# Performance work log

Measured on AMD Instinct MI355X. Metric: run time of the kernel, lower is better.

Reference implementation:

```python
import jax, jax.numpy as jnp
import numpy as np

D_MODEL = 1024
D_STATE = 128
HEADDIM = 64
EXPAND = 2
CHUNK = 64
D_CONV = 4
D_INNER = EXPAND * D_MODEL          # 2048
NHEADS = D_INNER // HEADDIM         # 32
D_IN_PROJ = 2 * D_INNER + 2 * D_STATE + NHEADS  # 4384
CONV_CH = D_INNER + 2 * D_STATE     # 2304
EPS = 1e-5


def segsum(x):
    # x: (..., T) -> (..., T, T); out[i, j] = sum_{k=j+1..i} x[k] for i>=j else -inf
    T = x.shape[-1]
    m1 = jnp.tril(jnp.ones((T, T), bool), -1)
    xr = jnp.where(m1, x[..., :, None], 0.0)   # zero above/at diagonal before cumsum
    s = jnp.cumsum(xr, axis=-2)
    m0 = jnp.tril(jnp.ones((T, T), bool), 0)
    return jnp.where(m0, s, -jnp.inf)


def ssd(x, A, B, C, chunk):
    # x: (b, L, h, p); A: (b, L, h); B, C: (b, L, n)  (the h=1 dim of the torch code is squeezed)
    b, L, h, p = x.shape
    c = L // chunk
    x = x.reshape(b, c, chunk, h, p)
    A = A.reshape(b, c, chunk, h).transpose(0, 3, 1, 2)  # (b, h, c, l)
    B = B.reshape(b, c, chunk, -1)                       # (b, c, l, n)
    C = C.reshape(b, c, chunk, -1)
    A_cum = jnp.cumsum(A, axis=-1)                       # (b, h, c, l)
    Lm = jnp.exp(segsum(A))                              # (b, h, c, l, l)
    # intra-chunk (diagonal block) output
    Y_diag = jnp.einsum('bcln,bcsn,bhcls,bcshp->bclhp', C, B, Lm, x)
    # per-chunk states
    decay_states = jnp.exp(A_cum[:, :, :, -1:] - A_cum)  # (b, h, c, l)
    states = jnp.einsum('bcln,bhcl,bclhp->bchpn', B, decay_states, x)
    init = jnp.zeros_like(states[:, :1])
    states = jnp.concatenate([init, states], axis=1)     # (b, c+1, h, p, n)
    # inter-chunk recurrence
    Ac_last = jnp.pad(A_cum[:, :, :, -1], ((0, 0), (0, 0), (1, 0)))  # (b, h, c+1)
    decay_chunk = jnp.exp(segsum(Ac_last))               # (b, h, c+1, c+1)
    new_states = jnp.einsum('bhzc,bchpn->bzhpn', decay_chunk, states)
    states = new_states[:, :-1]                          # (b, c, h, p, n)
    sdo = jnp.exp(A_cum)
    Y_off = jnp.einsum('bcln,bchpn,bhcl->bclhp', C, states, sdo)
    return (Y_diag + Y_off).reshape(b, L, h, p)


def setup_inputs() -> dict:
    key = jax.random.key(0)
    ks = jax.random.split(key, 8)
    return {
        'u': jax.random.normal(ks[0], (2, 4096, D_MODEL), jnp.float32),
        'W_in': jax.random.normal(ks[1], (D_MODEL, D_IN_PROJ), jnp.float32) * 0.02,
        'conv_w': jax.random.normal(ks[2], (CONV_CH, D_CONV), jnp.float32) * 0.3,
        'conv_b': jax.random.normal(ks[3], (CONV_CH,), jnp.float32) * 0.1,
        'dt_bias': jax.random.normal(ks[4], (NHEADS,), jnp.float32),
        'A_log': jax.random.normal(ks[5], (NHEADS,), jnp.float32) * 0.5,
        'D': jax.random.normal(ks[6], (NHEADS,), jnp.float32),
        'norm_w': jnp.ones((D_INNER,), jnp.float32),
        'W_out': jax.random.normal(ks[7], (D_INNER, D_MODEL), jnp.float32) * 0.02,
    }


def reference(u, W_in, conv_w, conv_b, dt_bias, A_log, D, norm_w, W_out):
    b, L, _ = u.shape
    zxbcdt = u @ W_in                                    # (b, L, 4384)
    z = zxbcdt[..., :D_INNER]
    xBC = zxbcdt[..., D_INNER:D_INNER + CONV_CH]
    dt = jax.nn.softplus(zxbcdt[..., -NHEADS:] + dt_bias)  # (b, L, h)
    # depthwise causal conv (Conv1d pad=d_conv-1, truncated to L == left-pad only)
    xc = jnp.pad(xBC.transpose(0, 2, 1), ((0, 0), (0, 0), (D_CONV - 1, 0)))
    xc = jax.lax.conv_general_dilated(
        xc, conv_w[:, None, :], (1,), 'VALID',
        feature_group_count=CONV_CH,
        dimension_numbers=('NCH', 'OIH', 'NCH')) + conv_b[None, :, None]
    xBC = jax.nn.silu(xc.transpose(0, 2, 1))             # (b, L, 2304)
    x = xBC[..., :D_INNER].reshape(b, L, NHEADS, HEADDIM)
    B = xBC[..., D_INNER:D_INNER + D_STATE]
    C = xBC[..., D_INNER + D_STATE:]
    A = -jnp.exp(A_log)                                  # (h,)
    y = ssd(x * dt[..., None], A * dt, B, C, CHUNK)
    y = y + x * D[:, None]
    y = y.reshape(b, L, D_INNER)
    # RMSNorm with gate z
    y = y * jax.nn.silu(z)
    y = y * jax.lax.rsqrt(jnp.mean(y * y, axis=-1, keepdims=True) + EPS) * norm_w
    return y @ W_out
```

## Files before the change

kernel.cpp:

```cpp
#include <hip/hip_runtime.h>
#include <hip/hip_bf16.h>
#include <math.h>

#define D_MODEL   1024
#define D_STATE   128
#define HEADDIM   64
#define CHUNK     64
#define D_INNER   2048
#define NHEADS    32
#define D_IN_PROJ 4384
#define CONV_CH   2304
#define RCOLS     2336
#define WINT_ROWS 4480
#define BATCH     2
#define SEQ       4096
#define NCHUNK    64
#define ROWS      (BATCH*SEQ)
#define EPS_RMS   1e-5f

typedef __hip_bfloat16 bf16;
typedef __bf16 bf16x8_t __attribute__((ext_vector_type(8)));
typedef float  f32x4_t  __attribute__((ext_vector_type(4)));

__device__ __forceinline__ float siluf_(float x){ return x/(1.f+expf(-x)); }
__device__ __forceinline__ float ldf(const float* p){ return *p; }
__device__ __forceinline__ float ldf(const bf16* p){ return __bfloat162float(*p); }
__device__ __forceinline__ void  stf(float* p, float v){ *p = v; }
__device__ __forceinline__ void  stf(bf16* p, float v){ *p = __float2bfloat16(v); }

__device__ __forceinline__ __bf16 tobf(float v){
    __hip_bfloat16 t = __float2bfloat16(v);
    return *reinterpret_cast<__bf16*>(&t);
}
__device__ __forceinline__ unsigned short bfbits(float v){
    __hip_bfloat16 t = __float2bfloat16(v);
    return *reinterpret_cast<unsigned short*>(&t);
}
__device__ __forceinline__ float bfbits2f(unsigned short u){
    union { unsigned u; float f; } cv; cv.u = ((unsigned)u) << 16; return cv.f;
}

__device__ __forceinline__ void async16(const void* g, void* l) {
    __builtin_amdgcn_global_load_lds(
        (const __attribute__((address_space(1))) unsigned int*)g,
        (__attribute__((address_space(3))) unsigned int*)l, 16, 0, 0);
}

struct Core {
    f32x4_t acc[4][4];

    __device__ __forceinline__ void stageA(const bf16* __restrict__ A, int lda,
                                           int row0, int kk, __bf16* Asb,
                                           int tid, int lcb, int wb) {
#pragma unroll
        for (int c = 0; c < 4; ++c) {
            const char* src = (const char*)(A + (size_t)(row0 + c * 64 + (tid >> 3)) * lda + kk) + lcb;
            async16(src, Asb + c * 4096 + wb);
        }
    }
    __device__ __forceinline__ void stageB(const bf16* __restrict__ Bt, int ldb,
                                           int col0, int kk, __bf16* Bsb,
                                           int tid, int lcb, int wb) {
#pragma unroll
        for (int c = 0; c < 2; ++c) {
            const char* src = (const char*)(Bt + (size_t)(col0 + c * 64 + (tid >> 3)) * ldb + kk) + lcb;
            async16(src, Bsb + c * 4096 + wb);
        }
    }

    __device__ __forceinline__ void run(const bf16* __restrict__ A,
                                        const bf16* __restrict__ Bt,
                                        int lda, int ldb,
                                        int row0, int col0, int k0, int nt,
                                        __bf16* As, __bf16* Bs, int tid) {
        const int wave = tid >> 6, lane = tid & 63;
        const int quad = lane >> 4, l16 = lane & 15;
        const int wm = wave >> 1, wn = wave & 1;
        const int wb  = wave << 9;
        const int lcb = (((tid & 7) ^ ((tid >> 3) & 7)) << 4);
        const int xb = (l16 & 7) << 4;

#pragma unroll
        for (int i = 0; i < 4; ++i)
#pragma unroll
            for (int j = 0; j < 4; ++j) acc[i][j] = (f32x4_t){0.f, 0.f, 0.f, 0.f};

        int aoff[4][2], boff[4][2];
#pragma unroll
        for (int mi = 0; mi < 4; ++mi)
#pragma unroll
            for (int ks = 0; ks < 2; ++ks) {
                const int cb = ((ks << 6) | (quad << 4)) ^ xb;
                aoff[mi][ks] = (wm * 64 + mi * 16 + l16) * 128 + cb;
                boff[mi][ks] = (wn * 64 + mi * 16 + l16) * 128 + cb;
            }

        stageA(A, lda, row0, k0,      As,          tid, lcb, wb);
        stageB(Bt, ldb, col0, k0,     Bs,          tid, lcb, wb);
        stageA(A, lda, row0, k0 + 64, As + 16384,  tid, lcb, wb);
        stageB(Bt, ldb, col0, k0 + 64, Bs + 8192,  tid, lcb, wb);

        const char* AsC = (const char*)As;
        const char* BsC = (const char*)Bs;
        int cur = 0, sb = 2;
        for (int t = 0; t < nt; ++t) {
            if (t < nt - 1) asm volatile("s_waitcnt vmcnt(6)" ::: "memory");
            else            asm volatile("s_waitcnt vmcnt(0)" ::: "memory");
            __builtin_amdgcn_s_barrier();
            asm volatile("" ::: "memory");
            if (t + 2 < nt) {
                stageA(A, lda, row0, k0 + (t + 2) * 64, As + sb * 16384, tid, lcb, wb);
                stageB(Bt, ldb, col0, k0 + (t + 2) * 64, Bs + sb * 8192, tid, lcb, wb);
            }
            const char* Ab = AsC + cur * 32768;
            const char* Bb = BsC + cur * 16384;
            bf16x8_t af[4][2], bfr[4][2];
#pragma unroll
            for (int mi = 0; mi < 4; ++mi)
#pragma unroll
                for (int ks = 0; ks < 2; ++ks) {
                    af[mi][ks]  = *(const bf16x8_t*)(Ab + aoff[mi][ks]);
                    bfr[mi][ks] = *(const bf16x8_t*)(Bb + boff[mi][ks]);
                }
            __builtin_amdgcn_s_setprio(1);
#pragma unroll
            for (int ks = 0; ks < 2; ++ks)
#pragma unroll
                for (int mi = 0; mi < 4; ++mi)
#pragma unroll
                    for (int ni = 0; ni < 4; ++ni)
                        acc[mi][ni] = __builtin_amdgcn_mfma_f32_16x16x32_bf16(
                            af[mi][ks], bfr[ni][ks], acc[mi][ni], 0, 0, 0);
            __builtin_amdgcn_s_setprio(0);
            cur = (cur + 1 == 3) ? 0 : cur + 1;
            sb  = (sb  + 1 == 3) ? 0 : sb  + 1;
        }
    }
};

__global__ __launch_bounds__(512) void gemm_zr_fused(const bf16* __restrict__ A,
                                                     const bf16* __restrict__ Bt,
                                                     bf16* __restrict__ Z,
                                                     bf16* __restrict__ R) {
    __shared__ __align__(16) __bf16 As[3 * 16384];
    __shared__ __align__(16) __bf16 Bs[3 * 8192];
    const int tid = threadIdx.x;
    const int row0 = blockIdx.x * 256;
    const int ct   = blockIdx.y;
    Core g;
    g.run(A, Bt, D_MODEL, D_MODEL, row0, ct * 128, 0, 16, As, Bs, tid);

    const int wave = tid >> 6, lane = tid & 63;
    const int quad = lane >> 4, l16 = lane & 15;
    const int wm = wave >> 1, wn = wave & 1;
    bf16* Cp; int ldc_, cl0, ncols;
    if (ct < 16) { Cp = Z; ldc_ = D_INNER; cl0 = ct * 128;           ncols = D_INNER; }
    else         { Cp = R; ldc_ = RCOLS;   cl0 = ct * 128 - D_INNER; ncols = RCOLS; }
#pragma unroll
    for (int ni = 0; ni < 4; ++ni) {
        int gc = cl0 + wn * 64 + ni * 16 + l16;
        if (gc >= ncols) continue;
#pragma unroll
        for (int mi = 0; mi < 4; ++mi)
#pragma unroll
            for (int r = 0; r < 4; ++r) {
                int gr = row0 + wm * 64 + mi * 16 + quad * 4 + r;
                stf(&Cp[(size_t)gr * ldc_ + gc], g.acc[mi][ni][r]);
            }
    }
}

__global__ __launch_bounds__(512) void gemm_out_kernel(const bf16* __restrict__ A,
                                                       const bf16* __restrict__ Bt,
                                                       float* __restrict__ out) {
    __shared__ __align__(16) __bf16 As[3 * 16384];
    __shared__ __align__(16) __bf16 Bs[3 * 8192];
    const int tid = threadIdx.x;
    const int row0 = blockIdx.x * 256;
    const int col0 = blockIdx.y * 128;
    Core g;
    g.run(A, Bt, D_INNER, D_INNER, row0, col0, 0, 32, As, Bs, tid);

    const int wave = tid >> 6, lane = tid & 63;
    const int quad = lane >> 4, l16 = lane & 15;
    const int wm = wave >> 1, wn = wave & 1;
#pragma unroll
    for (int ni = 0; ni < 4; ++ni) {
        int gc = col0 + wn * 64 + ni * 16 + l16;
#pragma unroll
        for (int mi = 0; mi < 4; ++mi)
#pragma unroll
            for (int r = 0; r < 4; ++r) {
                int gr = row0 + wm * 64 + mi * 16 + quad * 4 + r;
                out[(size_t)gr * D_MODEL + gc] = g.acc[mi][ni][r];
            }
    }
}

__global__ void cvt_bf16_kernel(const float* __restrict__ src,
                                bf16* __restrict__ dst, int n4) {
    int i = blockIdx.x * 256 + threadIdx.x;
    if (i >= n4) return;
    float4 v = ((const float4*)src)[i];
    dst[i * 4 + 0] = __float2bfloat16(v.x);
    dst[i * 4 + 1] = __float2bfloat16(v.y);
    dst[i * 4 + 2] = __float2bfloat16(v.z);
    dst[i * 4 + 3] = __float2bfloat16(v.w);
}

__global__ __launch_bounds__(256) void transpose_cvt_kernel(const float* __restrict__ W,
                                                            bf16* __restrict__ Wt,
                                                            int R, int C, int Cpad) {
    __shared__ float tile[32][33];
    int c0 = blockIdx.x * 32, r0 = blockIdx.y * 32;
    int tx = threadIdx.x & 31, ty = threadIdx.x >> 5;
    for (int i = ty; i < 32; i += 8) {
        int r = r0 + i, c = c0 + tx;
        tile[i][tx] = (c < C) ? W[(size_t)r * C + c] : 0.f;
    }
    __syncthreads();
    for (int i = ty; i < 32; i += 8) {
        int c = c0 + i, r = r0 + tx;
        stf(&Wt[(size_t)c * R + r], tile[tx][i]);
    }
}

__global__ void prep_convw_kernel(const float* __restrict__ conv_w,
                                  bf16* __restrict__ Wc) {
    int i = blockIdx.x * 256 + threadIdx.x;
    if (i >= CONV_CH * 4) return;
    int ch = i >> 2, k = i & 3;
    Wc[k * CONV_CH + ch] = __float2bfloat16(conv_w[ch * 4 + k]);
}

__global__ __launch_bounds__(256) void conv_silu_kernel(const bf16* __restrict__ R,
                                                        const bf16* __restrict__ Wc,
                                                        const float* __restrict__ conv_b,
                                                        bf16* __restrict__ xBC) {
    int idx = blockIdx.x * 256 + threadIdx.x;
    int rq = idx / 288;
    int g = idx - rq * 288;
    int ch0 = g * 8;
    int row0 = rq * 4;
    int l0 = row0 & (SEQ - 1);

    uint4 rv[7];
#pragma unroll
    for (int j = 0; j < 7; ++j) {
        int ls = l0 - 3 + j;
        rv[j] = (ls >= 0) ? *(const uint4*)&R[(size_t)(row0 - 3 + j) * RCOLS + ch0]
                          : make_uint4(0u, 0u, 0u, 0u);
    }
    uint4 wv[4];
#pragma unroll
    for (int k = 0; k < 4; ++k)
        wv[k] = *(const uint4*)&Wc[k * CONV_CH + ch0];
    float4 b0 = ((const float4*)conv_b)[ch0 / 4];
    float4 b1 = ((const float4*)conv_b)[ch0 / 4 + 1];
    const float bias[8] = {b0.x, b0.y, b0.z, b0.w, b1.x, b1.y, b1.z, b1.w};
    float wf[4][8];
#pragma unroll
    for (int k = 0; k < 4; ++k) {
        const unsigned* wp = (const unsigned*)&wv[k];
#pragma unroll
        for (int j2 = 0; j2 < 4; ++j2) {
            wf[k][2 * j2]     = bfbits2f((unsigned short)(wp[j2] & 0xffff));
            wf[k][2 * j2 + 1] = bfbits2f((unsigned short)(wp[j2] >> 16));
        }
    }
#pragma unroll
    for (int j = 0; j < 4; ++j) {
        float acc[8];
#pragma unroll
        for (int cc = 0; cc < 8; ++cc) acc[cc] = bias[cc];
#pragma unroll
        for (int k = 0; k < 4; ++k) {
            const unsigned* vp = (const unsigned*)&rv[j + k];
#pragma unroll
            for (int j2 = 0; j2 < 4; ++j2) {
                unsigned v = vp[j2];
                acc[2 * j2]     += wf[k][2 * j2]     * bfbits2f((unsigned short)(v & 0xffff));
                acc[2 * j2 + 1] += wf[k][2 * j2 + 1] * bfbits2f((unsigned short)(v >> 16));
            }
        }
        unsigned o[4];
#pragma unroll
        for (int j2 = 0; j2 < 4; ++j2)
            o[j2] = (unsigned)bfbits(siluf_(acc[2 * j2])) |
                    ((unsigned)bfbits(siluf_(acc[2 * j2 + 1])) << 16);
        *(uint4*)&xBC[(size_t)(row0 + j) * CONV_CH + ch0] = make_uint4(o[0], o[1], o[2], o[3]);
    }
}

__global__ void dt_kernel(const bf16* __restrict__ R,
                          const float* __restrict__ dt_bias,
                          float* __restrict__ dtb) {
    int i = blockIdx.x * 256 + threadIdx.x;
    int row = i >> 2, h0 = (i & 3) * 8;
    uint4 v = *(const uint4*)&R[(size_t)row * RCOLS + CONV_CH + h0];
    float4 bia0 = ((const float4*)dt_bias)[h0 / 4];
    float4 bia1 = ((const float4*)dt_bias)[h0 / 4 + 1];
    const unsigned vv[4] = {v.x, v.y, v.z, v.w};
    const float bb[8] = {bia0.x, bia0.y, bia0.z, bia0.w, bia1.x, bia1.y, bia1.z, bia1.w};
    float o[8];
#pragma unroll
    for (int j = 0; j < 4; ++j) {
        float a = bfbits2f((unsigned short)(vv[j] & 0xffff)) + bb[2*j];
        float c = bfbits2f((unsigned short)(vv[j] >> 16)) + bb[2*j+1];
        o[2*j]   = (a > 20.f) ? a : log1pf(expf(a));
        o[2*j+1] = (c > 20.f) ? c : log1pf(expf(c));
    }
    float* dp = &dtb[(size_t)row * NHEADS + h0];
    *(float4*)dp       = make_float4(o[0], o[1], o[2], o[3]);
    *(float4*)(dp + 4) = make_float4(o[4], o[5], o[6], o[7]);
}

__global__ void acum_kernel(const float* __restrict__ dtb,
                            const float* __restrict__ A_log,
                            float* __restrict__ Acum) {
    int bch = blockIdx.x;
    int h = bch & 31;
    int bc = bch >> 5;
    int c = bc & 63, b = bc >> 6;
    int row0 = b * SEQ + c * CHUNK;
    __shared__ float sh[64];
    int l = threadIdx.x;
    float Ah = -expf(A_log[h]);
    sh[l] = Ah * dtb[(size_t)(row0 + l) * NHEADS + h];
    __syncthreads();
    float s = 0.f;
    for (int j = 0; j <= l; ++j) s += sh[j];
    Acum[(size_t)bch * 64 + l] = s;
}

__global__ __launch_bounds__(64) void gchunk_mfma_kernel(const bf16* __restrict__ xBC,
                                                         float* __restrict__ Gbuf) {
    int bc = blockIdx.x;
    int c = bc & 63, b = bc >> 6;
    int row0 = b * SEQ + c * CHUNK;
    int lane = threadIdx.x;
    int quad = lane >> 4, l16 = lane & 15;

    f32x4_t acc[4][4];
#pragma unroll
    for (int i = 0; i < 4; ++i)
#pragma unroll
        for (int j = 0; j < 4; ++j) acc[i][j] = (f32x4_t){0.f, 0.f, 0.f, 0.f};

#pragma unroll
    for (int ks = 0; ks < 4; ++ks) {
        bf16x8_t a[4], bb[4];
#pragma unroll
        for (int mi = 0; mi < 4; ++mi)
            a[mi] = *(const bf16x8_t*)&xBC[(size_t)(row0 + mi * 16 + l16) * CONV_CH +
                                           D_INNER + D_STATE + ks * 32 + quad * 8];
#pragma unroll
        for (int ni = 0; ni < 4; ++ni)
            bb[ni] = *(const bf16x8_t*)&xBC[(size_t)(row0 + ni * 16 + l16) * CONV_CH +
                                            D_INNER + ks * 32 + quad * 8];
#pragma unroll
        for (int mi = 0; mi < 4; ++mi)
#pragma unroll
            for (int ni = 0; ni < 4; ++ni)
                acc[mi][ni] = __builtin_amdgcn_mfma_f32_16x16x32_bf16(
                    a[mi], bb[ni], acc[mi][ni], 0, 0, 0);
    }
#pragma unroll
    for (int ni = 0; ni < 4; ++ni) {
        int s = ni * 16 + l16;
#pragma unroll
        for (int mi = 0; mi < 4; ++mi)
#pragma unroll
            for (int r = 0; r < 4; ++r) {
                int l = mi * 16 + quad * 4 + r;
                Gbuf[(size_t)bc * 4096 + l * 64 + s] = acc[mi][ni][r];
            }
    }
}

__global__ __launch_bounds__(256) void states_mfma_kernel(const bf16* __restrict__ xBC,
                                                          const float* __restrict__ dtb,
                                                          const float* __restrict__ Acum,
                                                          bf16* __restrict__ states) {
    __shared__ __align__(16) __bf16 BsT[128 * 72];
    __shared__ __align__(16) __bf16 xdT[4][64 * 72];
    __shared__ float dtdec[4][64];
    int bcq = blockIdx.x;
    int hq = bcq & 7, bc = bcq >> 3;
    int c = bc & 63, b = bc >> 6;
    int tid = threadIdx.x, wave = tid >> 6, lane = tid & 63;
    int h = hq * 4 + wave;
    int bch = bc * 32 + h;
    int row0 = b * SEQ + c * CHUNK;
    int quad = lane >> 4, l16 = lane & 15;

    {
        float alast = Acum[(size_t)bch * 64 + 63];
        float a = Acum[(size_t)bch * 64 + lane];
        dtdec[wave][lane] = dtb[(size_t)(row0 + lane) * NHEADS + h] * expf(alast - a);
    }
    __syncthreads();
    for (int it = 0; it < 16; ++it) {
        int i2 = tid + 256 * it;
        int l = i2 >> 6;
        int n0 = (i2 & 63) * 2;
        unsigned v = *(const unsigned*)&xBC[(size_t)(row0 + l) * CONV_CH + D_INNER + n0];
        *(unsigned short*)&BsT[(n0    ) * 72 + l] = (unsigned short)(v & 0xffff);
        *(unsigned short*)&BsT[(n0 + 1) * 72 + l] = (unsigned short)(v >> 16);
    }
    for (int it = 0; it < 32; ++it) {
        int l = 2 * it + (lane >> 5);
        int p0 = (lane & 31) * 2;
        unsigned v = *(const unsigned*)&xBC[(size_t)(row0 + l) * CONV_CH + h * 64 + p0];
        float f = dtdec[wave][l];
        xdT[wave][(p0    ) * 72 + l] = tobf(bfbits2f((unsigned short)(v & 0xffff)) * f);
        xdT[wave][(p0 + 1) * 72 + l] = tobf(bfbits2f((unsigned short)(v >> 16)) * f);
    }
    __syncthreads();

    f32x4_t acc[4][8];
#pragma unroll
    for (int i = 0; i < 4; ++i)
#pragma unroll
        for (int j = 0; j < 8; ++j) acc[i][j] = (f32x4_t){0.f, 0.f, 0.f, 0.f};
#pragma unroll
    for (int ks = 0; ks < 2; ++ks) {
        bf16x8_t a[4], bb[8];
#pragma unroll
        for (int mi = 0; mi < 4; ++mi)
            a[mi] = *(const bf16x8_t*)(&xdT[wave][(mi * 16 + l16) * 72 + ks * 32 + quad * 8]);
#pragma unroll
        for (int ni = 0; ni < 8; ++ni)
            bb[ni] = *(const bf16x8_t*)(&BsT[(ni * 16 + l16) * 72 + ks * 32 + quad * 8]);
#pragma unroll
        for (int mi = 0; mi < 4; ++mi)
#pragma unroll
            for (int ni = 0; ni < 8; ++ni)
                acc[mi][ni] = __builtin_amdgcn_mfma_f32_16x16x32_bf16(
                    a[mi], bb[ni], acc[mi][ni], 0, 0, 0);
    }
#pragma unroll
    for (int ni = 0; ni < 8; ++ni) {
        int n = ni * 16 + l16;
#pragma unroll
        for (int mi = 0; mi < 4; ++mi)
#pragma unroll
            for (int r = 0; r < 4; ++r) {
                int p = mi * 16 + quad * 4 + r;
                stf(&states[(size_t)bch * 8192 + p * 128 + n], acc[mi][ni][r]);
            }
    }
}

__global__ void scan_kernel(const float* __restrict__ Acum,
                            bf16* __restrict__ states) {
    int i = blockIdx.x * 256 + threadIdx.x;
    int pn0 = (i & 2047) * 4;
    int bh = i >> 11;
    int h = bh & 31, b = bh >> 5;
    float carry[4] = {0.f, 0.f, 0.f, 0.f};
    for (int c = 0; c < NCHUNK; ++c) {
        int bch = (b * NCHUNK + c) * NHEADS + h;
        bf16* sp = &states[(size_t)bch * 8192 + pn0];
        uint2 v = *(const uint2*)sp;
        float s0 = bfbits2f((unsigned short)(v.x & 0xffff));
        float s1 = bfbits2f((unsigned short)(v.x >> 16));
        float s2 = bfbits2f((unsigned short)(v.y & 0xffff));
        float s3 = bfbits2f((unsigned short)(v.y >> 16));
        uint2 o;
        o.x = (unsigned)bfbits(carry[0]) | ((unsigned)bfbits(carry[1]) << 16);
        o.y = (unsigned)bfbits(carry[2]) | ((unsigned)bfbits(carry[3]) << 16);
        *(uint2*)sp = o;
        float dec = expf(Acum[(size_t)bch * 64 + 63]);
        carry[0] = carry[0] * dec + s0;
        carry[1] = carry[1] * dec + s1;
        carry[2] = carry[2] * dec + s2;
        carry[3] = carry[3] * dec + s3;
    }
}

__global__ __launch_bounds__(64) void y_mfma_kernel(const bf16* __restrict__ xBC,
                                                    const float* __restrict__ dtb,
                                                    const float* __restrict__ Acum,
                                                    const float* __restrict__ Gbuf,
                                                    const bf16* __restrict__ states,
                                                    const float* __restrict__ Dv,
                                                    bf16* __restrict__ y) {
    __shared__ __align__(16) __bf16 Mm[64 * 72];
    __shared__ __align__(16) __bf16 xsT[64 * 72];
    __shared__ float acs[64], dtss[64], sdos[64];
    int bch = blockIdx.x;
    int h = bch & 31, bc = bch >> 5;
    int c = bc & 63, b = bc >> 6;
    int row0 = b * SEQ + c * CHUNK;
    int lane = threadIdx.x;
    int quad = lane >> 4, l16 = lane & 15;

    {
        float a = Acum[(size_t)bch * 64 + lane];
        acs[lane] = a;
        sdos[lane] = expf(a);
        dtss[lane] = dtb[(size_t)(row0 + lane) * NHEADS + h];
    }
    __syncthreads();
    for (int l = 0; l < 64; ++l) {
        int s = lane;
        float d = acs[l] - acs[s];
        float g = (s <= l) ? Gbuf[(size_t)bc * 4096 + l * 64 + s] * dtss[s] : 0.f;
        float coef = g * expf((s <= l) ? d : 0.f);
        Mm[l * 72 + s] = tobf(coef);
    }
    for (int it = 0; it < 32; ++it) {
        int l = 2 * it + (lane >> 5);
        int p0 = (lane & 31) * 2;
        unsigned v = *(const unsigned*)&xBC[(size_t)(row0 + l) * CONV_CH + h * 64 + p0];
        *(unsigned short*)&xsT[(p0    ) * 72 + l] = (unsigned short)(v & 0xffff);
        *(unsigned short*)&xsT[(p0 + 1) * 72 + l] = (unsigned short)(v >> 16);
    }
    __syncthreads();

    f32x4_t acc[4][4];
#pragma unroll
    for (int i = 0; i < 4; ++i)
#pragma unroll
        for (int j = 0; j < 4; ++j) acc[i][j] = (f32x4_t){0.f, 0.f, 0.f, 0.f};

#pragma unroll
    for (int ks = 0; ks < 2; ++ks) {
        bf16x8_t a[4], bb[4];
#pragma unroll
        for (int mi = 0; mi < 4; ++mi)
            a[mi] = *(const bf16x8_t*)(&Mm[(mi * 16 + l16) * 72 + ks * 32 + quad * 8]);
#pragma unroll
        for (int ni = 0; ni < 4; ++ni)
            bb[ni] = *(const bf16x8_t*)(&xsT[(ni * 16 + l16) * 72 + ks * 32 + quad * 8]);
#pragma unroll
        for (int mi = 0; mi < 4; ++mi)
#pragma unroll
            for (int ni = 0; ni < 4; ++ni)
                acc[mi][ni] = __builtin_amdgcn_mfma_f32_16x16x32_bf16(
                    a[mi], bb[ni], acc[mi][ni], 0, 0, 0);
    }
    float sdo_mi[4];
#pragma unroll
    for (int mi = 0; mi < 4; ++mi) sdo_mi[mi] = sdos[mi * 16 + l16];
#pragma unroll
    for (int ks = 0; ks < 4; ++ks) {
        bf16x8_t a[4], bb[4];
#pragma unroll
        for (int mi = 0; mi < 4; ++mi) {
            const unsigned* cp = (const unsigned*)&xBC[(size_t)(row0 + mi * 16 + l16) * CONV_CH
                                                       + D_INNER + D_STATE + ks * 32 + quad * 8];
            float sc = sdo_mi[mi];
#pragma unroll
            for (int jj = 0; jj < 4; ++jj) {
                unsigned v = cp[jj];
                a[mi][2 * jj    ] = tobf(bfbits2f((unsigned short)(v & 0xffff)) * sc);
                a[mi][2 * jj + 1] = tobf(bfbits2f((unsigned short)(v >> 16)) * sc);
            }
        }
#pragma unroll
        for (int ni = 0; ni < 4; ++ni)
            bb[ni] = *(const bf16x8_t*)&states[(size_t)bch * 8192 + (ni * 16 + l16) * 128
                                               + ks * 32 + quad * 8];
#pragma unroll
        for (int mi = 0; mi < 4; ++mi)
#pragma unroll
            for (int ni = 0; ni < 4; ++ni)
                acc[mi][ni] = __builtin_amdgcn_mfma_f32_16x16x32_bf16(
                    a[mi], bb[ni], acc[mi][ni], 0, 0, 0);
    }
    float Dh = Dv[h];
#pragma unroll
    for (int ni = 0; ni < 4; ++ni) {
        int p = ni * 16 + l16;
#pragma unroll
        for (int mi = 0; mi < 4; ++mi)
#pragma unroll
            for (int r = 0; r < 4; ++r) {
                int l = mi * 16 + quad * 4 + r;
                float xv = bfbits2f(*(const unsigned short*)&xsT[p * 72 + l]);
                stf(&y[(size_t)(row0 + l) * D_INNER + h * 64 + p],
                    acc[mi][ni][r] + Dh * xv);
            }
    }
}

__global__ __launch_bounds__(256) void gate_norm_kernel(const bf16* __restrict__ Z,
                                                        const float* __restrict__ nw,
                                                        bf16* __restrict__ y) {
    int row = blockIdx.x;
    int tid = threadIdx.x;
    int col0 = tid * 8;
    uint4 zv = *(const uint4*)&Z[(size_t)row * D_INNER + col0];
    uint4 yv = *(const uint4*)&y[(size_t)row * D_INNER + col0];
    const unsigned zz[4] = {zv.x, zv.y, zv.z, zv.w};
    const unsigned yy[4] = {yv.x, yv.y, yv.z, yv.w};
    float vals[8];
    float local = 0.f;
#pragma unroll
    for (int j = 0; j < 4; ++j) {
        float z0 = bfbits2f((unsigned short)(zz[j] & 0xffff));
        float z1 = bfbits2f((unsigned short)(zz[j] >> 16));
        float y0 = bfbits2f((unsigned short)(yy[j] & 0xffff));
        float y1 = bfbits2f((unsigned short)(yy[j] >> 16));
        float v0 = y0 * siluf_(z0);
        float v1 = y1 * siluf_(z1);
        vals[2*j] = v0; vals[2*j+1] = v1;
        local += v0 * v0 + v1 * v1;
    }
#pragma unroll
    for (int off = 32; off; off >>= 1) local += __shfl_down(local, off, 64);
    __shared__ float wsum[4];
    if ((tid & 63) == 0) wsum[tid >> 6] = local;
    __syncthreads();
    float total = wsum[0] + wsum[1] + wsum[2] + wsum[3];
    float scale = rsqrtf(total / (float)D_INNER + EPS_RMS);
    float4 w0 = ((const float4*)nw)[col0 / 4];
    float4 w1 = ((const float4*)nw)[col0 / 4 + 1];
    const float ww[8] = {w0.x, w0.y, w0.z, w0.w, w1.x, w1.y, w1.z, w1.w};
    unsigned o[4];
#pragma unroll
    for (int j = 0; j < 4; ++j)
        o[j] = (unsigned)bfbits(vals[2*j] * scale * ww[2*j]) |
               ((unsigned)bfbits(vals[2*j+1] * scale * ww[2*j+1]) << 16);
    *(uint4*)&y[(size_t)row * D_INNER + col0] = make_uint4(o[0], o[1], o[2], o[3]);
}

extern "C" void kernel_launch(void* const* d_in, const int* in_sizes, int n_in,
                              void* d_out, int out_size, void* d_ws, size_t ws_size,
                              hipStream_t stream) {
    const float* u       = (const float*)d_in[0];
    const float* W_in    = (const float*)d_in[1];
    const float* conv_w  = (const float*)d_in[2];
    const float* conv_b  = (const float*)d_in[3];
    const float* dt_bias = (const float*)d_in[4];
    const float* A_log   = (const float*)d_in[5];
    const float* Dv      = (const float*)d_in[6];
    const float* norm_w  = (const float*)d_in[7];
    const float* W_out   = (const float*)d_in[8];
    float* out = (float*)d_out;

    const size_t sz_xBC    = (size_t)ROWS * CONV_CH * 2;
    const size_t sz_Z      = (size_t)ROWS * D_INNER * 2;
    const size_t sz_y      = (size_t)ROWS * D_INNER * 2;
    const size_t sz_states = (size_t)BATCH * NCHUNK * NHEADS * 8192 * 2;
    const size_t sz_dtb    = (size_t)ROWS * NHEADS * 4;
    const size_t sz_Acum   = (size_t)BATCH * NCHUNK * NHEADS * 64 * 4;
    const size_t sz_Gbuf   = (size_t)BATCH * NCHUNK * 4096 * 4;
    const size_t sz_WinT   = (size_t)WINT_ROWS * D_MODEL * 2;
    const size_t sz_WoutT  = (size_t)D_MODEL * D_INNER * 2;
    const size_t sz_Wc     = (size_t)CONV_CH * 4 * 2;
    const size_t need = sz_xBC + sz_Z + sz_y + sz_states + sz_dtb + sz_Acum +
                        sz_Gbuf + sz_WinT + sz_WoutT + sz_Wc;
    if (ws_size < need) {
        hipMemsetAsync(d_out, 0, (size_t)out_size * sizeof(float), stream);
        return;
    }
    char* ws = (char*)d_ws;
    size_t off = 0;
    bf16*  xBC    = (bf16*) (ws + off); off += sz_xBC;
    bf16*  Z      = (bf16*) (ws + off); off += sz_Z;
    bf16*  y      = (bf16*) (ws + off); off += sz_y;
    bf16*  states = (bf16*) (ws + off); off += sz_states;
    float* dtb    = (float*)(ws + off); off += sz_dtb;
    float* Acum   = (float*)(ws + off); off += sz_Acum;
    float* Gbuf   = (float*)(ws + off); off += sz_Gbuf;
    bf16*  W_inT  = (bf16*) (ws + off); off += sz_WinT;
    bf16*  W_outT = (bf16*) (ws + off); off += sz_WoutT;
    bf16*  Wc     = (bf16*) (ws + off); off += sz_Wc;
    bf16*  R        = states;
    bf16*  u_bf16   = (bf16*)((char*)states + (size_t)ROWS * RCOLS * 2);

    cvt_bf16_kernel<<<(ROWS * D_MODEL / 4 + 255) / 256, 256, 0, stream>>>(
        u, u_bf16, ROWS * D_MODEL / 4);
    transpose_cvt_kernel<<<dim3(WINT_ROWS / 32, D_MODEL / 32), 256, 0, stream>>>(
        W_in, W_inT, D_MODEL, D_IN_PROJ, WINT_ROWS);
    transpose_cvt_kernel<<<dim3(D_MODEL / 32, D_INNER / 32), 256, 0, stream>>>(
        W_out, W_outT, D_INNER, D_MODEL, D_MODEL);
    prep_convw_kernel<<<(CONV_CH * 4 + 255) / 256, 256, 0, stream>>>(conv_w, Wc);
    gemm_zr_fused<<<dim3(ROWS / 256, 35), 512, 0, stream>>>(u_bf16, W_inT, Z, R);
    conv_silu_kernel<<<ROWS / 4 * 288 / 256, 256, 0, stream>>>(R, Wc, conv_b, xBC);
    dt_kernel<<<ROWS * 4 / 256, 256, 0, stream>>>(R, dt_bias, dtb);
    acum_kernel<<<BATCH * NCHUNK * NHEADS, 64, 0, stream>>>(dtb, A_log, Acum);
    gchunk_mfma_kernel<<<BATCH * NCHUNK, 64, 0, stream>>>(xBC, Gbuf);
    states_mfma_kernel<<<BATCH * NCHUNK * 8, 256, 0, stream>>>(xBC, dtb, Acum, states);
    scan_kernel<<<BATCH * NHEADS * 2048 / 256, 256, 0, stream>>>(Acum, states);
    y_mfma_kernel<<<BATCH * NCHUNK * NHEADS, 64, 0, stream>>>(
        xBC, dtb, Acum, Gbuf, states, Dv, y);
    gate_norm_kernel<<<ROWS, 256, 0, stream>>>(Z, norm_w, y);
    gemm_out_kernel<<<dim3(ROWS / 256, D_MODEL / 128), 512, 0, stream>>>(
        y, W_outT, out);
}
```

Measured before the change: 445.1 us.

## Interleave GEMM LDS fragment loads, async staging and MFMA in quarter phases

```diff
diff --git a/kernel.cpp b/kernel.cpp
--- a/kernel.cpp
+++ b/kernel.cpp
@@ -49,18 +49,18 @@
 struct Core {
     f32x4_t acc[4][4];
 
-    __device__ __forceinline__ void stageA(const bf16* __restrict__ A, int lda,
-                                           int row0, int kk, __bf16* Asb,
-                                           int tid, int lcb, int wb) {
-#pragma unroll
-        for (int c = 0; c < 4; ++c) {
+    __device__ __forceinline__ void stA2(const bf16* __restrict__ A, int lda,
+                                         int row0, int kk, __bf16* Asb,
+                                         int tid, int lcb, int wb, int c0) {
+#pragma unroll
+        for (int c = c0; c < c0 + 2; ++c) {
             const char* src = (const char*)(A + (size_t)(row0 + c * 64 + (tid >> 3)) * lda + kk) + lcb;
             async16(src, Asb + c * 4096 + wb);
         }
     }
-    __device__ __forceinline__ void stageB(const bf16* __restrict__ Bt, int ldb,
-                                           int col0, int kk, __bf16* Bsb,
-                                           int tid, int lcb, int wb) {
+    __device__ __forceinline__ void stB2(const bf16* __restrict__ Bt, int ldb,
+                                         int col0, int kk, __bf16* Bsb,
+                                         int tid, int lcb, int wb) {
 #pragma unroll
         for (int c = 0; c < 2; ++c) {
             const char* src = (const char*)(Bt + (size_t)(col0 + c * 64 + (tid >> 3)) * ldb + kk) + lcb;
@@ -95,45 +95,100 @@
                 boff[mi][ks] = (wn * 64 + mi * 16 + l16) * 128 + cb;
             }
 
-        stageA(A, lda, row0, k0,      As,          tid, lcb, wb);
-        stageB(Bt, ldb, col0, k0,     Bs,          tid, lcb, wb);
-        stageA(A, lda, row0, k0 + 64, As + 16384,  tid, lcb, wb);
-        stageB(Bt, ldb, col0, k0 + 64, Bs + 8192,  tid, lcb, wb);
+        stA2(A, lda, row0, k0, As, tid, lcb, wb, 0);
+        stA2(A, lda, row0, k0, As, tid, lcb, wb, 2);
+        stB2(Bt, ldb, col0, k0, Bs, tid, lcb, wb);
+        stA2(A, lda, row0, k0 + 64, As + 16384, tid, lcb, wb, 0);
+        stA2(A, lda, row0, k0 + 64, As + 16384, tid, lcb, wb, 2);
+        stB2(Bt, ldb, col0, k0 + 64, Bs + 8192, tid, lcb, wb);
 
         const char* AsC = (const char*)As;
         const char* BsC = (const char*)Bs;
-        int cur = 0, sb = 2;
+        int cur = 0;
         for (int t = 0; t < nt; ++t) {
             if (t < nt - 1) asm volatile("s_waitcnt vmcnt(6)" ::: "memory");
             else            asm volatile("s_waitcnt vmcnt(0)" ::: "memory");
             __builtin_amdgcn_s_barrier();
             asm volatile("" ::: "memory");
-            if (t + 2 < nt) {
-                stageA(A, lda, row0, k0 + (t + 2) * 64, As + sb * 16384, tid, lcb, wb);
-                stageB(Bt, ldb, col0, k0 + (t + 2) * 64, Bs + sb * 8192, tid, lcb, wb);
-            }
+
+            const int sb = (cur + 2 >= 3) ? cur - 1 : cur + 2;
+            const bool st = (t + 2 < nt);
+            const int kk = k0 + (t + 2) * 64;
             const char* Ab = AsC + cur * 32768;
             const char* Bb = BsC + cur * 16384;
-            bf16x8_t af[4][2], bfr[4][2];
-#pragma unroll
-            for (int mi = 0; mi < 4; ++mi)
+            __bf16* Asb = As + sb * 16384;
+            __bf16* Bsb = Bs + sb * 8192;
+
+            bf16x8_t af0[2][2], af1[2][2], bf0[2][2], bf1[2][2];
+
+#pragma unroll
+            for (int i = 0; i < 2; ++i)
 #pragma unroll
                 for (int ks = 0; ks < 2; ++ks) {
-                    af[mi][ks]  = *(const bf16x8_t*)(Ab + aoff[mi][ks]);
-                    bfr[mi][ks] = *(const bf16x8_t*)(Bb + boff[mi][ks]);
+                    af0[i][ks] = *(const bf16x8_t*)(Ab + aoff[i][ks]);
+                    bf0[i][ks] = *(const bf16x8_t*)(Bb + boff[i][ks]);
                 }
+            if (st) stA2(A, lda, row0, kk, Asb, tid, lcb, wb, 0);
+            asm volatile("" ::: "memory");
+            __builtin_amdgcn_s_barrier();
+            asm volatile("" ::: "memory");
             __builtin_amdgcn_s_setprio(1);
 #pragma unroll
             for (int ks = 0; ks < 2; ++ks)
 #pragma unroll
-                for (int mi = 0; mi < 4; ++mi)
-#pragma unroll
-                    for (int ni = 0; ni < 4; ++ni)
+                for (int mi = 0; mi < 2; ++mi)
+#pragma unroll
+                    for (int ni = 0; ni < 2; ++ni)
                         acc[mi][ni] = __builtin_amdgcn_mfma_f32_16x16x32_bf16(
-                            af[mi][ks], bfr[ni][ks], acc[mi][ni], 0, 0, 0);
+                            af0[mi][ks], bf0[ni][ks], acc[mi][ni], 0, 0, 0);
             __builtin_amdgcn_s_setprio(0);
+
+#pragma unroll
+            for (int i = 0; i < 2; ++i)
+#pragma unroll
+                for (int ks = 0; ks < 2; ++ks)
+                    bf1[i][ks] = *(const bf16x8_t*)(Bb + boff[2 + i][ks]);
+            if (st) stA2(A, lda, row0, kk, Asb, tid, lcb, wb, 2);
+            asm volatile("" ::: "memory");
+            __builtin_amdgcn_s_barrier();
+            asm volatile("" ::: "memory");
+            __builtin_amdgcn_s_setprio(1);
+#pragma unroll
+            for (int ks = 0; ks < 2; ++ks)
+#pragma unroll
+                for (int mi = 0; mi < 2; ++mi)
+#pragma unroll
+                    for (int ni = 0; ni < 2; ++ni)
+                        acc[mi][2 + ni] = __builtin_amdgcn_mfma_f32_16x16x32_bf16(
+                            af0[mi][ks], bf1[ni][ks], acc[mi][2 + ni], 0, 0, 0);
+            __builtin_amdgcn_s_setprio(0);
+
+#pragma unroll
+            for (int i = 0; i < 2; ++i)
+#pragma unroll
+                for (int ks = 0; ks < 2; ++ks)
+                    af1[i][ks] = *(const bf16x8_t*)(Ab + aoff[2 + i][ks]);
+            if (st) stB2(Bt, ldb, col0, kk, Bsb, tid, lcb, wb);
+            asm volatile("" ::: "memory");
+            __builtin_amdgcn_s_barrier();
+            asm volatile("" ::: "memory");
+            __builtin_amdgcn_s_setprio(1);
+#pragma unroll
+            for (int ks = 0; ks < 2; ++ks)
+#pragma unroll
+                for (int mi = 0; mi < 2; ++mi) {
+#pragma unroll
+                    for (int ni = 0; ni < 2; ++ni)
+                        acc[2 + mi][2 + ni] = __builtin_amdgcn_mfma_f32_16x16x32_bf16(
+                            af1[mi][ks], bf1[ni][ks], acc[2 + mi][2 + ni], 0, 0, 0);
+#pragma unroll
+                    for (int ni = 0; ni < 2; ++ni)
+                        acc[2 + mi][ni] = __builtin_amdgcn_mfma_f32_16x16x32_bf16(
+                            af1[mi][ks], bf0[ni][ks], acc[2 + mi][ni], 0, 0, 0);
+                }
+            __builtin_amdgcn_s_setprio(0);
+
             cur = (cur + 1 == 3) ? 0 : cur + 1;
-            sb  = (sb  + 1 == 3) ? 0 : sb  + 1;
         }
     }
 };
```

Result: no change. 437.4 us (-1.7%).
